# Kernel optimization log

Measured on AMD Instinct MI355X. Metric: run time of the kernel, lower is better.

The kernel has to match this reference:

```python
import jax, jax.numpy as jnp
import numpy as np
from jax import lax

KSIZE = 3
SIGMA = 0.8
BLOCK = 8
DCT_THRESH = 2.5
DCT_CLIP = 10.0
DWT_LAM = 0.05


def _gaussian_kernel(dtype):
    coords = jnp.arange(KSIZE, dtype=dtype) - (KSIZE - 1) / 2.0
    grid = coords[None, :] ** 2 + coords[:, None] ** 2
    k = jnp.exp(-grid / (2.0 * SIGMA * SIGMA))
    return k / k.sum()


def gaussian_blur(x):
    # depthwise 3x3 gaussian with reflect padding, groups=C
    C = x.shape[1]
    k = _gaussian_kernel(x.dtype)
    kernel = jnp.broadcast_to(k[None, None], (C, 1, KSIZE, KSIZE))
    pad = KSIZE // 2
    xp = jnp.pad(x, ((0, 0), (0, 0), (pad, pad), (pad, pad)), mode='reflect')
    return lax.conv_general_dilated(
        xp, kernel, window_strides=(1, 1), padding='VALID',
        dimension_numbers=('NCHW', 'OIHW', 'NCHW'), feature_group_count=C)


def block_dct_normalize(x):
    # 8x8 block "DCT" implemented (as in the source) via fft2().real, then
    # soft shrink of small coeffs + clip, then ifft2().real reconstruction.
    B, C, H, W = x.shape
    Ph, Pw = H // BLOCK, W // BLOCK  # H, W chosen as multiples of 8 -> no pad
    blocks = x.reshape(B, C, Ph, BLOCK, Pw, BLOCK).transpose(0, 1, 2, 4, 3, 5)
    coeff = jnp.fft.fft2(blocks, norm='ortho').real
    ca = jnp.abs(coeff)
    coeff = jnp.where(ca < DCT_THRESH, coeff * (ca / (DCT_THRESH + 1e-8)), coeff)
    coeff = jnp.clip(coeff, -DCT_CLIP, DCT_CLIP)
    rec = jnp.fft.ifft2(coeff.astype(jnp.complex64), norm='ortho').real
    rec = rec.transpose(0, 1, 2, 4, 3, 5).reshape(B, C, H, W)
    return rec.astype(x.dtype)


def haar_dwt2(x):
    # orthonormal 2x2 Haar analysis; sign/order conventions cancel in the
    # soft-threshold + inverse pipeline (soft_threshold is odd in sign)
    B, C, H, W = x.shape
    r = x.reshape(B, C, H // 2, 2, W // 2, 2)
    a, b = r[:, :, :, 0, :, 0], r[:, :, :, 0, :, 1]
    c, d = r[:, :, :, 1, :, 0], r[:, :, :, 1, :, 1]
    LL = (a + b + c + d) * 0.5
    LH = (a + b - c - d) * 0.5
    HL = (a - b + c - d) * 0.5
    HH = (a - b - c + d) * 0.5
    return LL, LH, HL, HH


def haar_idwt2(LL, LH, HL, HH):
    B, C, Hh, Wh = LL.shape
    a = (LL + LH + HL + HH) * 0.5
    b = (LL + LH - HL - HH) * 0.5
    c = (LL - LH + HL - HH) * 0.5
    d = (LL - LH - HL + HH) * 0.5
    top = jnp.stack([a, b], axis=-1)  # (B,C,Hh,Wh,2)
    bot = jnp.stack([c, d], axis=-1)
    r = jnp.stack([top, bot], axis=3)  # (B,C,Hh,2,Wh,2)
    return r.reshape(B, C, 2 * Hh, 2 * Wh)


def soft_threshold(x, lam):
    return jnp.sign(x) * jnp.maximum(jnp.abs(x) - lam, 0.0)


def wavelet_refine(x):
    LL, LH, HL, HH = haar_dwt2(x)
    return haar_idwt2(LL, soft_threshold(LH, DWT_LAM),
                      soft_threshold(HL, DWT_LAM),
                      soft_threshold(HH, DWT_LAM))


def setup_inputs() -> dict:
    key = jax.random.key(0)
    I = jax.random.uniform(key, (32, 3, 512, 512), dtype=jnp.float32)
    return {"I": I}


def reference(I):
    I_g = gaussian_blur(I)
    I_d = block_dct_normalize(I_g)
    R_d = I_g - I_d
    I_d_wave = wavelet_refine(I_d)
    R_d_wave = wavelet_refine(R_d)
    # input_mode='concat', residual_type='R_d'
    return jnp.concatenate([I_d_wave, R_d_wave], axis=1)
```

## Files before the change

### kernel.cpp

```cpp
#include <hip/hip_runtime.h>

#define HW 512

__device__ __forceinline__ int reflect512(int v) {
    v = v < 0 ? -v : v;
    v = v > 511 ? 1022 - v : v;
    return v;
}

__device__ __forceinline__ float softt(float x) {
    return copysignf(fmaxf(fabsf(x) - 0.05f, 0.0f), x);
}

__device__ __forceinline__ void haar_quad(float a, float b, float c, float d,
                                          float& oa, float& ob, float& oc, float& od) {
    float LL = (a + b + c + d) * 0.5f;
    float LH = (a + b - c - d) * 0.5f;
    float HL = (a - b + c - d) * 0.5f;
    float HH = (a - b - c + d) * 0.5f;
    LH = softt(LH); HL = softt(HL); HH = softt(HH);
    oa = (LL + LH + HL + HH) * 0.5f;
    ob = (LL + LH - HL - HH) * 0.5f;
    oc = (LL - LH + HL - HH) * 0.5f;
    od = (LL - LH - HL + HH) * 0.5f;
}

#define RA 0.35355339059327373f
#define RB 0.25f

__device__ __forceinline__ void dft8_cos(const float* __restrict__ x, float* __restrict__ P) {
    float e0 = x[0] + x[4], d0 = x[0] - x[4];
    float e1 = x[2] + x[6];
    float o0 = x[1] + x[5], m0 = x[1] - x[5];
    float o1 = x[3] + x[7], m1 = x[3] - x[7];
    float see = e0 + e1, dee = e0 - e1, soo = o0 + o1;
    float dd = m0 - m1;
    P[0] = RA * (see + soo);
    P[4] = RA * (see - soo);
    float p2 = RA * dee;
    P[2] = p2; P[6] = p2;
    float t0 = RA * d0, t1 = RB * dd;
    P[1] = t0 + t1; P[7] = t0 + t1;
    P[3] = t0 - t1; P[5] = t0 - t1;
}

__device__ __forceinline__ void dft8_sin(const float* __restrict__ x, float* __restrict__ Q) {
    float d1 = x[2] - x[6];
    float o0 = x[1] + x[5], m0 = x[1] - x[5];
    float o1 = x[3] + x[7], m1 = x[3] - x[7];
    float qq = m0 + m1;
    Q[0] = 0.0f; Q[4] = 0.0f;
    float q2 = RA * (o0 - o1);
    Q[2] = q2; Q[6] = -q2;
    float t0 = RB * qq, t1 = RA * d1;
    Q[1] = t0 + t1; Q[7] = -(t0 + t1);
    Q[3] = t0 - t1; Q[5] = -(t0 - t1);
}

__launch_bounds__(256, 2)
__global__ void sas_fused(const float* __restrict__ in, float* __restrict__ out) {
    const int lane = threadIdx.x & 63;
    const int wv = threadIdx.x >> 6;
    const int p = blockIdx.y;
    const int by = blockIdx.x * 4 + wv;
    const float* __restrict__ inP = in + (size_t)p * (HW * HW);
    const int cx = lane * 8;

    float4 va[10], vb[10];
#pragma unroll
    for (int j = 0; j < 10; ++j) {
        int gy = reflect512(by * 8 - 1 + j);
        const float* r = inP + (size_t)gy * HW + cx;
        va[j] = *(const float4*)r;
        vb[j] = *(const float4*)(r + 4);
    }

    float x[10][10];
#pragma unroll
    for (int j = 0; j < 10; ++j) {
        float lft = __shfl_up(vb[j].w, 1);
        float rgt = __shfl_down(va[j].x, 1);
        if (lane == 0)  lft = va[j].y;
        if (lane == 63) rgt = vb[j].z;
        x[j][0] = lft;
        x[j][1] = va[j].x; x[j][2] = va[j].y; x[j][3] = va[j].z; x[j][4] = va[j].w;
        x[j][5] = vb[j].x; x[j][6] = vb[j].y; x[j][7] = vb[j].z; x[j][8] = vb[j].w;
        x[j][9] = rgt;
    }

    const float e = 0.45783336f;
    const float inv_s = 1.0f / ((1.0f + 2.0f * e) * (1.0f + 2.0f * e));
    float B[8][8];
#pragma unroll
    for (int j = 0; j < 8; ++j) {
        float v[10];
#pragma unroll
        for (int c = 0; c < 10; ++c)
            v[c] = e * (x[j][c] + x[j + 2][c]) + x[j + 1][c];
#pragma unroll
        for (int c = 0; c < 8; ++c)
            B[j][c] = (e * (v[c] + v[c + 2]) + v[c + 1]) * inv_s;
    }

    float P[8][8], Q[8][8];
#pragma unroll
    for (int m = 0; m < 8; ++m) { dft8_cos(B[m], P[m]); dft8_sin(B[m], Q[m]); }
#pragma unroll
    for (int v = 0; v < 8; ++v) {
        float pc[8], qc[8], tc[8], sc[8];
#pragma unroll
        for (int m = 0; m < 8; ++m) { pc[m] = P[m][v]; qc[m] = Q[m][v]; }
        dft8_cos(pc, tc);
        dft8_sin(qc, sc);
#pragma unroll
        for (int u = 0; u < 8; ++u) {
            float t = tc[u] - sc[u];
            float ca = fabsf(t);
            t = (ca < 2.5f) ? t * (ca * 0.4f) : t;
            t = fminf(fmaxf(t, -10.0f), 10.0f);
            P[u][v] = t;
        }
    }
#pragma unroll
    for (int m = 0; m < 8; ++m) {
        float tr[8];
#pragma unroll
        for (int n = 0; n < 8; ++n) tr[n] = P[m][n];
        dft8_cos(tr, P[m]);
        dft8_sin(tr, Q[m]);
    }
#pragma unroll
    for (int v = 0; v < 8; ++v) {
        float pc[8], qc[8], tc[8], sc[8];
#pragma unroll
        for (int m = 0; m < 8; ++m) { pc[m] = P[m][v]; qc[m] = Q[m][v]; }
        dft8_cos(pc, tc);
        dft8_sin(qc, sc);
#pragma unroll
        for (int u = 0; u < 8; ++u) P[u][v] = tc[u] - sc[u];
    }

    const int chId = (p / 3) * 6 + (p % 3);
    float* __restrict__ oI = out + ((size_t)chId << 18);
    float* __restrict__ oR = out + ((size_t)(chId + 3) << 18);
#pragma unroll
    for (int qy = 0; qy < 4; ++qy) {
        float ti[2][8], tr_[2][8];
#pragma unroll
        for (int qx = 0; qx < 4; ++qx) {
            float d00 = P[2*qy][2*qx],   d01 = P[2*qy][2*qx+1];
            float d10 = P[2*qy+1][2*qx], d11 = P[2*qy+1][2*qx+1];
            haar_quad(d00, d01, d10, d11,
                      ti[0][2*qx], ti[0][2*qx+1], ti[1][2*qx], ti[1][2*qx+1]);
            float r00 = B[2*qy][2*qx]   - d00, r01 = B[2*qy][2*qx+1]   - d01;
            float r10 = B[2*qy+1][2*qx] - d10, r11 = B[2*qy+1][2*qx+1] - d11;
            haar_quad(r00, r01, r10, r11,
                      tr_[0][2*qx], tr_[0][2*qx+1], tr_[1][2*qx], tr_[1][2*qx+1]);
        }
        size_t base = (size_t)(by * 8 + 2 * qy) * HW + cx;
        *(float4*)&oI[base]          = make_float4(ti[0][0], ti[0][1], ti[0][2], ti[0][3]);
        *(float4*)&oI[base + 4]      = make_float4(ti[0][4], ti[0][5], ti[0][6], ti[0][7]);
        *(float4*)&oI[base + HW]     = make_float4(ti[1][0], ti[1][1], ti[1][2], ti[1][3]);
        *(float4*)&oI[base + HW + 4] = make_float4(ti[1][4], ti[1][5], ti[1][6], ti[1][7]);
        *(float4*)&oR[base]          = make_float4(tr_[0][0], tr_[0][1], tr_[0][2], tr_[0][3]);
        *(float4*)&oR[base + 4]      = make_float4(tr_[0][4], tr_[0][5], tr_[0][6], tr_[0][7]);
        *(float4*)&oR[base + HW]     = make_float4(tr_[1][0], tr_[1][1], tr_[1][2], tr_[1][3]);
        *(float4*)&oR[base + HW + 4] = make_float4(tr_[1][4], tr_[1][5], tr_[1][6], tr_[1][7]);
    }
}

extern "C" void kernel_launch(void* const* d_in, const int* in_sizes, int n_in,
                              void* d_out, int out_size, void* d_ws, size_t ws_size,
                              hipStream_t stream) {
    const float* I = (const float*)d_in[0];
    float* out = (float*)d_out;
    dim3 grid(16, 96);
    sas_fused<<<grid, dim3(256), 0, stream>>>(I, out);
}
```

Before: 279.3 us.

## Use packed real-FFT for block DFT and stream separable blur per row

Replaces the separate cos/sin 8-point DFT passes with a packed real-FFT layout. Conjugate-symmetric columns are processed in pairs, so the real/imaginary arrays P and Q collapse into a single 8x8 array and register pressure drops. The horizontal blur is now computed row by row into a rolling 3-row buffer, and the row FFT is fused right after each blurred row. Launch bounds are raised to 3 blocks per CU and outputs use nontemporal stores; the risks are register spills at the higher occupancy target and errors in the permuted index bookkeeping.

```diff
diff --git a/kernel.cpp b/kernel.cpp
--- a/kernel.cpp
+++ b/kernel.cpp
@@ -1,6 +1,10 @@
 #include <hip/hip_runtime.h>
 
 #define HW 512
+#define RA 0.35355339059327373f
+#define RB 0.25f
+
+typedef float fx4 __attribute__((ext_vector_type(4)));
 
 __device__ __forceinline__ int reflect512(int v) {
     v = v < 0 ? -v : v;
@@ -25,39 +29,89 @@
     od = (LL - LH - HL + HH) * 0.5f;
 }
 
-#define RA 0.35355339059327373f
-#define RB 0.25f
-
-__device__ __forceinline__ void dft8_cos(const float* __restrict__ x, float* __restrict__ P) {
+__device__ __forceinline__ void rfft8(const float* __restrict__ x, float* __restrict__ o) {
+    float e0 = x[0] + x[4], d0 = x[0] - x[4];
+    float e1 = x[2] + x[6], d1 = x[2] - x[6];
+    float o0 = x[1] + x[5], m0 = x[1] - x[5];
+    float o1 = x[3] + x[7], m1 = x[3] - x[7];
+    float see = e0 + e1, dee = e0 - e1, soo = o0 + o1;
+    float dd = m0 - m1, qq = m0 + m1;
+    o[0] = RA * (see + soo);
+    o[4] = RA * (see - soo);
+    o[2] = RA * dee;
+    float t0 = RA * d0, t1 = RB * dd;
+    o[1] = t0 + t1;
+    o[3] = t0 - t1;
+    float u0 = RB * qq, u1 = RA * d1;
+    o[5] = u0 + u1;
+    o[6] = RA * (o0 - o1);
+    o[7] = u0 - u1;
+}
+
+__device__ __forceinline__ void dft8_cos(const float* __restrict__ x, float* __restrict__ t) {
     float e0 = x[0] + x[4], d0 = x[0] - x[4];
     float e1 = x[2] + x[6];
     float o0 = x[1] + x[5], m0 = x[1] - x[5];
     float o1 = x[3] + x[7], m1 = x[3] - x[7];
     float see = e0 + e1, dee = e0 - e1, soo = o0 + o1;
     float dd = m0 - m1;
-    P[0] = RA * (see + soo);
-    P[4] = RA * (see - soo);
+    t[0] = RA * (see + soo);
+    t[4] = RA * (see - soo);
     float p2 = RA * dee;
-    P[2] = p2; P[6] = p2;
-    float t0 = RA * d0, t1 = RB * dd;
-    P[1] = t0 + t1; P[7] = t0 + t1;
-    P[3] = t0 - t1; P[5] = t0 - t1;
-}
-
-__device__ __forceinline__ void dft8_sin(const float* __restrict__ x, float* __restrict__ Q) {
+    t[2] = p2; t[6] = p2;
+    float a0 = RA * d0, a1 = RB * dd;
+    t[1] = a0 + a1; t[7] = a0 + a1;
+    t[3] = a0 - a1; t[5] = a0 - a1;
+}
+
+__device__ __forceinline__ void dft8_sin(const float* __restrict__ x, float* __restrict__ t) {
     float d1 = x[2] - x[6];
     float o0 = x[1] + x[5], m0 = x[1] - x[5];
     float o1 = x[3] + x[7], m1 = x[3] - x[7];
     float qq = m0 + m1;
-    Q[0] = 0.0f; Q[4] = 0.0f;
+    t[0] = 0.0f; t[4] = 0.0f;
     float q2 = RA * (o0 - o1);
-    Q[2] = q2; Q[6] = -q2;
-    float t0 = RB * qq, t1 = RA * d1;
-    Q[1] = t0 + t1; Q[7] = -(t0 + t1);
-    Q[3] = t0 - t1; Q[5] = -(t0 - t1);
-}
-
-__launch_bounds__(256, 2)
+    t[2] = q2; t[6] = -q2;
+    float a0 = RB * qq, a1 = RA * d1;
+    t[1] = a0 + a1; t[7] = -(a0 + a1);
+    t[3] = a0 - a1; t[5] = -(a0 - a1);
+}
+
+__device__ __forceinline__ float nonlin(float t) {
+    float ca = fabsf(t);
+    t = (ca < 2.5f) ? t * (ca * 0.4f) : t;
+    return fminf(fmaxf(t, -10.0f), 10.0f);
+}
+
+template <bool NL>
+__device__ __forceinline__ void colpass(float A[8][8]) {
+#pragma unroll
+    for (int v0 = 0; v0 <= 4; v0 += 4) {
+        float c[8], t[8];
+#pragma unroll
+        for (int m = 0; m < 8; ++m) c[m] = A[m][v0];
+        dft8_cos(c, t);
+#pragma unroll
+        for (int u = 0; u < 8; ++u) A[u][v0] = NL ? nonlin(t[u]) : t[u];
+    }
+#pragma unroll
+    for (int v = 1; v <= 3; ++v) {
+        float c[8], q[8], tc[8], ts[8];
+#pragma unroll
+        for (int m = 0; m < 8; ++m) { c[m] = A[m][v]; q[m] = A[m][4 + v]; }
+        dft8_cos(c, tc);
+        dft8_sin(q, ts);
+#pragma unroll
+        for (int u = 0; u < 8; ++u) {
+            float lo = tc[u] - ts[u];
+            float hi = tc[u] + ts[u];
+            A[u][v] = NL ? nonlin(lo) : lo;
+            A[u][4 + v] = NL ? nonlin(hi) : hi;
+        }
+    }
+}
+
+__launch_bounds__(256, 3)
 __global__ void sas_fused(const float* __restrict__ in, float* __restrict__ out) {
     const int lane = threadIdx.x & 63;
     const int wv = threadIdx.x >> 6;
@@ -66,80 +120,60 @@
     const float* __restrict__ inP = in + (size_t)p * (HW * HW);
     const int cx = lane * 8;
 
-    float4 va[10], vb[10];
+    const float e = 0.45783336f;
+    const float inv_s = 1.0f / ((1.0f + 2.0f * e) * (1.0f + 2.0f * e));
+
+    fx4 va[10], vb[10];
 #pragma unroll
     for (int j = 0; j < 10; ++j) {
         int gy = reflect512(by * 8 - 1 + j);
         const float* r = inP + (size_t)gy * HW + cx;
-        va[j] = *(const float4*)r;
-        vb[j] = *(const float4*)(r + 4);
-    }
-
-    float x[10][10];
+        va[j] = *(const fx4*)r;
+        vb[j] = *(const fx4*)(r + 4);
+    }
+
+    float h[3][8];
+    float B[8][8], A[8][8];
 #pragma unroll
     for (int j = 0; j < 10; ++j) {
         float lft = __shfl_up(vb[j].w, 1);
         float rgt = __shfl_down(va[j].x, 1);
         if (lane == 0)  lft = va[j].y;
         if (lane == 63) rgt = vb[j].z;
-        x[j][0] = lft;
-        x[j][1] = va[j].x; x[j][2] = va[j].y; x[j][3] = va[j].z; x[j][4] = va[j].w;
-        x[j][5] = vb[j].x; x[j][6] = vb[j].y; x[j][7] = vb[j].z; x[j][8] = vb[j].w;
-        x[j][9] = rgt;
-    }
-
-    const float e = 0.45783336f;
-    const float inv_s = 1.0f / ((1.0f + 2.0f * e) * (1.0f + 2.0f * e));
-    float B[8][8];
-#pragma unroll
-    for (int j = 0; j < 8; ++j) {
-        float v[10];
-#pragma unroll
-        for (int c = 0; c < 10; ++c)
-            v[c] = e * (x[j][c] + x[j + 2][c]) + x[j + 1][c];
-#pragma unroll
-        for (int c = 0; c < 8; ++c)
-            B[j][c] = (e * (v[c] + v[c + 2]) + v[c + 1]) * inv_s;
-    }
-
-    float P[8][8], Q[8][8];
-#pragma unroll
-    for (int m = 0; m < 8; ++m) { dft8_cos(B[m], P[m]); dft8_sin(B[m], Q[m]); }
-#pragma unroll
-    for (int v = 0; v < 8; ++v) {
-        float pc[8], qc[8], tc[8], sc[8];
-#pragma unroll
-        for (int m = 0; m < 8; ++m) { pc[m] = P[m][v]; qc[m] = Q[m][v]; }
-        dft8_cos(pc, tc);
-        dft8_sin(qc, sc);
-#pragma unroll
-        for (int u = 0; u < 8; ++u) {
-            float t = tc[u] - sc[u];
-            float ca = fabsf(t);
-            t = (ca < 2.5f) ? t * (ca * 0.4f) : t;
-            t = fminf(fmaxf(t, -10.0f), 10.0f);
-            P[u][v] = t;
+        float x0 = lft, x1 = va[j].x, x2 = va[j].y, x3 = va[j].z, x4 = va[j].w;
+        float x5 = vb[j].x, x6 = vb[j].y, x7 = vb[j].z, x8 = vb[j].w, x9 = rgt;
+        float* hj = h[j % 3];
+        hj[0] = e * (x0 + x2) + x1;
+        hj[1] = e * (x1 + x3) + x2;
+        hj[2] = e * (x2 + x4) + x3;
+        hj[3] = e * (x3 + x5) + x4;
+        hj[4] = e * (x4 + x6) + x5;
+        hj[5] = e * (x5 + x7) + x6;
+        hj[6] = e * (x6 + x8) + x7;
+        hj[7] = e * (x7 + x9) + x8;
+        if (j >= 2) {
+            const int r = j - 2;
+            const float* h0 = h[r % 3];
+            const float* h1 = h[(r + 1) % 3];
+            const float* h2 = h[(r + 2) % 3];
+#pragma unroll
+            for (int c = 0; c < 8; ++c)
+                B[r][c] = (e * (h0[c] + h2[c]) + h1[c]) * inv_s;
+            rfft8(B[r], A[r]);
         }
     }
+
+    colpass<true>(A);
+
 #pragma unroll
     for (int m = 0; m < 8; ++m) {
-        float tr[8];
-#pragma unroll
-        for (int n = 0; n < 8; ++n) tr[n] = P[m][n];
-        dft8_cos(tr, P[m]);
-        dft8_sin(tr, Q[m]);
-    }
-#pragma unroll
-    for (int v = 0; v < 8; ++v) {
-        float pc[8], qc[8], tc[8], sc[8];
-#pragma unroll
-        for (int m = 0; m < 8; ++m) { pc[m] = P[m][v]; qc[m] = Q[m][v]; }
-        dft8_cos(pc, tc);
-        dft8_sin(qc, sc);
-#pragma unroll
-        for (int u = 0; u < 8; ++u) P[u][v] = tc[u] - sc[u];
-    }
-
+        float x[8] = {A[m][0], A[m][1], A[m][2], A[m][3],
+                      A[m][4], A[m][7], A[m][6], A[m][5]};
+        rfft8(x, A[m]);
+    }
+    colpass<false>(A);
+
+    constexpr int SG[8] = {0, 1, 2, 3, 4, 7, 6, 5};
     const int chId = (p / 3) * 6 + (p % 3);
     float* __restrict__ oI = out + ((size_t)chId << 18);
     float* __restrict__ oR = out + ((size_t)(chId + 3) << 18);
@@ -148,8 +182,8 @@
         float ti[2][8], tr_[2][8];
 #pragma unroll
         for (int qx = 0; qx < 4; ++qx) {
-            float d00 = P[2*qy][2*qx],   d01 = P[2*qy][2*qx+1];
-            float d10 = P[2*qy+1][2*qx], d11 = P[2*qy+1][2*qx+1];
+            float d00 = A[2*qy][SG[2*qx]],   d01 = A[2*qy][SG[2*qx+1]];
+            float d10 = A[2*qy+1][SG[2*qx]], d11 = A[2*qy+1][SG[2*qx+1]];
             haar_quad(d00, d01, d10, d11,
                       ti[0][2*qx], ti[0][2*qx+1], ti[1][2*qx], ti[1][2*qx+1]);
             float r00 = B[2*qy][2*qx]   - d00, r01 = B[2*qy][2*qx+1]   - d01;
@@ -158,14 +192,23 @@
                       tr_[0][2*qx], tr_[0][2*qx+1], tr_[1][2*qx], tr_[1][2*qx+1]);
         }
         size_t base = (size_t)(by * 8 + 2 * qy) * HW + cx;
-        *(float4*)&oI[base]          = make_float4(ti[0][0], ti[0][1], ti[0][2], ti[0][3]);
-        *(float4*)&oI[base + 4]      = make_float4(ti[0][4], ti[0][5], ti[0][6], ti[0][7]);
-        *(float4*)&oI[base + HW]     = make_float4(ti[1][0], ti[1][1], ti[1][2], ti[1][3]);
-        *(float4*)&oI[base + HW + 4] = make_float4(ti[1][4], ti[1][5], ti[1][6], ti[1][7]);
-        *(float4*)&oR[base]          = make_float4(tr_[0][0], tr_[0][1], tr_[0][2], tr_[0][3]);
-        *(float4*)&oR[base + 4]      = make_float4(tr_[0][4], tr_[0][5], tr_[0][6], tr_[0][7]);
-        *(float4*)&oR[base + HW]     = make_float4(tr_[1][0], tr_[1][1], tr_[1][2], tr_[1][3]);
-        *(float4*)&oR[base + HW + 4] = make_float4(tr_[1][4], tr_[1][5], tr_[1][6], tr_[1][7]);
+        fx4 w;
+        w = (fx4){ti[0][0], ti[0][1], ti[0][2], ti[0][3]};
+        __builtin_nontemporal_store(w, (fx4*)&oI[base]);
+        w = (fx4){ti[0][4], ti[0][5], ti[0][6], ti[0][7]};
+        __builtin_nontemporal_store(w, (fx4*)&oI[base + 4]);
+        w = (fx4){ti[1][0], ti[1][1], ti[1][2], ti[1][3]};
+        __builtin_nontemporal_store(w, (fx4*)&oI[base + HW]);
+        w = (fx4){ti[1][4], ti[1][5], ti[1][6], ti[1][7]};
+        __builtin_nontemporal_store(w, (fx4*)&oI[base + HW + 4]);
+        w = (fx4){tr_[0][0], tr_[0][1], tr_[0][2], tr_[0][3]};
+        __builtin_nontemporal_store(w, (fx4*)&oR[base]);
+        w = (fx4){tr_[0][4], tr_[0][5], tr_[0][6], tr_[0][7]};
+        __builtin_nontemporal_store(w, (fx4*)&oR[base + 4]);
+        w = (fx4){tr_[1][0], tr_[1][1], tr_[1][2], tr_[1][3]};
+        __builtin_nontemporal_store(w, (fx4*)&oR[base + HW]);
+        w = (fx4){tr_[1][4], tr_[1][5], tr_[1][6], tr_[1][7]};
+        __builtin_nontemporal_store(w, (fx4*)&oR[base + HW + 4]);
     }
 }
 
```

Result: slower. 345.1 us (+23.5%).
